# Kernel optimization log

Hardware: AMD Instinct MI355X
Metric: run time of the kernel (lower is better)

Reference implementation:

```python
import jax, jax.numpy as jnp
import numpy as np

B, S, D, E, K = 4, 2048, 1024, 8, 2


def setup_inputs() -> dict:
    key = jax.random.key(0)
    k1, k2, k3 = jax.random.split(key, 3)
    scale = 1.0 / np.sqrt(D)
    x = jax.random.normal(k1, (B, S, D), dtype=jnp.float32)
    Wg = jax.random.normal(k2, (D, E), dtype=jnp.float32) * scale
    bg = jnp.zeros((E,), dtype=jnp.float32)
    We = jax.random.normal(k3, (E, D, D), dtype=jnp.float32) * scale
    be = jnp.zeros((E, D), dtype=jnp.float32)
    return {"x": x, "Wg": Wg, "bg": bg, "We": We, "be": be}


def reference(x, Wg, bg, We, be):
    # gate scores: [B, S, E]
    gate_scores = jnp.einsum("bsd,de->bse", x, Wg) + bg
    topk_values, topk_indices = jax.lax.top_k(gate_scores, K)
    # mask: -inf everywhere except at top-k indices (where value == score)
    sel = jax.nn.one_hot(topk_indices, E, dtype=jnp.bool_).any(axis=-2)  # [B,S,E]
    masked = jnp.where(sel, gate_scores, -jnp.inf)
    gate_weights = jax.nn.softmax(masked, axis=-1)  # [B,S,E]
    # dense all-expert compute, as in the original: [B,S,E,D]
    expert_outputs = jnp.einsum("bsd,edh->bseh", x, We) + be
    fused = jnp.einsum("bse,bseh->bsh", gate_weights, expert_outputs)
    return fused
```

## Files before the change

### kernel.cpp

```cpp
#include <hip/hip_runtime.h>
#include <stdint.h>

#define NTOK   8192
#define DIM    1024
#define NEXP   8
#define MAXP   8192

#define BM 128
#define BN 128
#define BK 32

typedef float  f32x4  __attribute__((ext_vector_type(4)));
typedef __bf16 bf16x8 __attribute__((ext_vector_type(8)));

typedef __attribute__((address_space(1))) const void* gas_ptr;
typedef __attribute__((address_space(3))) void*       las_ptr;

__device__ __forceinline__ unsigned short f32_to_bf16(float f) {
  union { float f; unsigned int u; } v; v.f = f;
  unsigned int u = v.u;
  unsigned int r = (u + 0x7FFFu + ((u >> 16) & 1u)) >> 16;
  return (unsigned short)r;
}

__global__ __launch_bounds__(256) void prep_kernel(
    const float* __restrict__ We, unsigned short* __restrict__ Wt,
    const float* __restrict__ x, const float* __restrict__ Wg,
    const float* __restrict__ bg, unsigned short* __restrict__ Xbf,
    int* __restrict__ tok_ee, float2* __restrict__ tok_w) {
  __shared__ float tile[64][65];
  const int bid = blockIdx.x;
  if (bid < 2048) {
    const int e  = bid >> 8;
    const int d0 = ((bid >> 4) & 15) * 64;
    const int h0 = (bid & 15) * 64;
    const int t  = threadIdx.x;
    const int tx = t & 63, ty = t >> 6;
    const float* src = We + (size_t)e * DIM * DIM;
#pragma unroll
    for (int i = 0; i < 16; ++i) {
      int d = ty + i * 4;
      tile[d][tx] = src[(size_t)(d0 + d) * DIM + (h0 + tx)];
    }
    __syncthreads();
    unsigned short* dst = Wt + (size_t)e * DIM * DIM;
    const int tx2 = t & 31, ty8 = t >> 5;
#pragma unroll
    for (int i = 0; i < 8; ++i) {
      int h = ty8 + i * 8;
      int d = tx2 * 2;
      unsigned int pk = (unsigned int)f32_to_bf16(tile[d][h]) |
                        ((unsigned int)f32_to_bf16(tile[d + 1][h]) << 16);
      *(unsigned int*)&dst[(size_t)(h0 + h) * DIM + d0 + d] = pk;
    }
    return;
  }
  const int blk  = bid - 2048;
  const int wave = threadIdx.x >> 6;
  const int lane = threadIdx.x & 63;
  const int tok0 = blk * 16 + wave * 4;

  float xs[4][16];
#pragma unroll
  for (int t = 0; t < 4; ++t) {
    const float* xr = x + (size_t)(tok0 + t) * DIM + lane * 16;
#pragma unroll
    for (int i = 0; i < 4; ++i)
      *(f32x4*)&xs[t][i * 4] = *(const f32x4*)(xr + i * 4);
  }
#pragma unroll
  for (int t = 0; t < 4; ++t) {
    unsigned int pk[8];
#pragma unroll
    for (int i = 0; i < 8; ++i)
      pk[i] = (unsigned int)f32_to_bf16(xs[t][2 * i]) |
              ((unsigned int)f32_to_bf16(xs[t][2 * i + 1]) << 16);
    uint4* xb = (uint4*)(Xbf + (size_t)(tok0 + t) * DIM + lane * 16);
    xb[0] = make_uint4(pk[0], pk[1], pk[2], pk[3]);
    xb[1] = make_uint4(pk[4], pk[5], pk[6], pk[7]);
  }

  double acc[4][8];
#pragma unroll
  for (int t = 0; t < 4; ++t)
#pragma unroll
    for (int e = 0; e < 8; ++e) acc[t][e] = 0.0;

  const float* wr = Wg + (size_t)(lane * 16) * NEXP;
#pragma unroll
  for (int i = 0; i < 16; ++i) {
    f32x4 wa = *(const f32x4*)(wr + i * 8);
    f32x4 wb = *(const f32x4*)(wr + i * 8 + 4);
    double w0 = wa[0], w1 = wa[1], w2 = wa[2], w3 = wa[3];
    double w4 = wb[0], w5 = wb[1], w6 = wb[2], w7 = wb[3];
#pragma unroll
    for (int t = 0; t < 4; ++t) {
      double xd = (double)xs[t][i];
      acc[t][0] += xd * w0; acc[t][1] += xd * w1;
      acc[t][2] += xd * w2; acc[t][3] += xd * w3;
      acc[t][4] += xd * w4; acc[t][5] += xd * w5;
      acc[t][6] += xd * w6; acc[t][7] += xd * w7;
    }
  }
#pragma unroll
  for (int m = 1; m < 64; m <<= 1)
#pragma unroll
    for (int t = 0; t < 4; ++t)
#pragma unroll
      for (int e = 0; e < 8; ++e) acc[t][e] += __shfl_xor(acc[t][e], m, 64);

  if (lane == 0) {
#pragma unroll
    for (int t = 0; t < 4; ++t) {
      float s[8];
#pragma unroll
      for (int e = 0; e < 8; ++e) s[e] = (float)acc[t][e] + bg[e];
      int i0 = 0; float v0 = s[0];
#pragma unroll
      for (int e = 1; e < 8; ++e) if (s[e] > v0) { v0 = s[e]; i0 = e; }
      int i1 = -1; float v1 = -3.4e38f;
#pragma unroll
      for (int e = 0; e < 8; ++e) if (e != i0 && s[e] > v1) { v1 = s[e]; i1 = e; }
      float t1 = expf(v1 - v0);
      float den = 1.0f + t1;
      tok_ee[tok0 + t] = i0 | (i1 << 8);
      tok_w[tok0 + t]  = make_float2(1.0f / den, t1 / den);
    }
  }
}

__global__ __launch_bounds__(1024) void compact_kernel(
    const int* __restrict__ tok_ee, const float2* __restrict__ tok_w,
    int* __restrict__ counts, int* __restrict__ pair_token,
    float* __restrict__ pair_w) {
  __shared__ int wave_cnt[16][NEXP];
  __shared__ int wave_off[16][NEXP];
  __shared__ int base[NEXP];
  __shared__ int chunk_tot[NEXP];
  const int tid = threadIdx.x, wave = tid >> 6, lane = tid & 63;
  if (tid < NEXP) base[tid] = 0;
  __syncthreads();
  for (int c = 0; c < NTOK / 1024; ++c) {
    const int t = c * 1024 + tid;
    const int p = tok_ee[t];
    const int e0 = p & 255, e1 = (p >> 8) & 255;
    const float2 w = tok_w[t];
    int pre0 = 0, pre1 = 0;
    const unsigned long long below = (1ull << lane) - 1ull;
#pragma unroll
    for (int e = 0; e < NEXP; ++e) {
      unsigned long long m = __ballot(e0 == e || e1 == e);
      if (e0 == e) pre0 = __popcll(m & below);
      if (e1 == e) pre1 = __popcll(m & below);
      if (lane == 0) wave_cnt[wave][e] = __popcll(m);
    }
    __syncthreads();
    if (tid < NEXP) {
      int s = 0;
      for (int w2 = 0; w2 < 16; ++w2) {
        wave_off[w2][tid] = s;
        s += wave_cnt[w2][tid];
      }
      chunk_tot[tid] = s;
    }
    __syncthreads();
    const int s0 = base[e0] + wave_off[wave][e0] + pre0;
    const int s1 = base[e1] + wave_off[wave][e1] + pre1;
    pair_token[e0 * MAXP + s0] = (t << 1);     pair_w[e0 * MAXP + s0] = w.x;
    pair_token[e1 * MAXP + s1] = (t << 1) | 1; pair_w[e1 * MAXP + s1] = w.y;
    __syncthreads();
    if (tid < NEXP) base[tid] += chunk_tot[tid];
    __syncthreads();
  }
  if (tid < NEXP) counts[tid] = base[tid];
}

__global__ __launch_bounds__(256) void moe_gemm(
    const unsigned short* __restrict__ Xbf, const unsigned short* __restrict__ Wt,
    const float* __restrict__ be, const int* __restrict__ counts,
    const int* __restrict__ pair_token, const float* __restrict__ pair_w,
    float* __restrict__ part, float* __restrict__ Y, int use_part) {
  const int id  = blockIdx.x;
  const int e   = id & 7;
  const int n0  = ((id >> 3) & 7) * BN;
  const int m0  = (id >> 6) * BM;
  const int cnt = counts[e];
  if (m0 >= cnt) return;

  __shared__ __align__(16) unsigned short As[2][BM * BK];
  __shared__ __align__(16) unsigned short Bs[2][BN * BK];

  const int tid  = threadIdx.x;
  const int wave = tid >> 6;
  const int lane = tid & 63;
  const int fm   = lane & 15;
  const int fq   = lane >> 4;
  const int wm   = wave >> 1;
  const int wn   = wave & 1;

  const int srow = wave * 32 + (lane >> 2);
  const int kc   = (lane & 3) * 8;
  const unsigned short* gA[2];
  const unsigned short* gB[2];
#pragma unroll
  for (int c = 0; c < 2; ++c) {
    int r  = srow + c * 16;
    int gr = m0 + r;
    int tk = (gr < cnt) ? (pair_token[e * MAXP + gr] >> 1) : 0;
    gA[c] = Xbf + (size_t)tk * DIM + kc;
    gB[c] = Wt + (size_t)e * DIM * DIM + (size_t)(n0 + r) * DIM + kc;
  }

#define STAGE(buf, koff)                                                      \
  {                                                                           \
    _Pragma("unroll") for (int c = 0; c < 2; ++c) {                           \
      __builtin_amdgcn_global_load_lds(                                       \
          (gas_ptr)(uintptr_t)(gA[c] + (koff)),                               \
          (las_ptr)(uintptr_t)(&As[buf][(wave * 2 + c) * 512]), 16, 0, 0);    \
      __builtin_amdgcn_global_load_lds(                                       \
          (gas_ptr)(uintptr_t)(gB[c] + (koff)),                               \
          (las_ptr)(uintptr_t)(&Bs[buf][(wave * 2 + c) * 512]), 16, 0, 0);    \
    }                                                                         \
  }

  f32x4 acc[4][4];
#pragma unroll
  for (int i = 0; i < 4; ++i)
#pragma unroll
    for (int j = 0; j < 4; ++j) { f32x4 z = {0.f, 0.f, 0.f, 0.f}; acc[i][j] = z; }

  STAGE(0, 0);
  int cur = 0;
  for (int k0 = 0; k0 < DIM; k0 += BK) {
    __syncthreads();
    if (k0 + BK < DIM) STAGE(cur ^ 1, k0 + BK);

    bf16x8 af[4], bfr[4];
#pragma unroll
    for (int i = 0; i < 4; ++i)
      af[i] = *(const bf16x8*)&As[cur][(wm * 64 + i * 16 + fm) * BK + fq * 8];
#pragma unroll
    for (int j = 0; j < 4; ++j)
      bfr[j] = *(const bf16x8*)&Bs[cur][(wn * 64 + j * 16 + fm) * BK + fq * 8];
#pragma unroll
    for (int i = 0; i < 4; ++i)
#pragma unroll
      for (int j = 0; j < 4; ++j)
        acc[i][j] = __builtin_amdgcn_mfma_f32_16x16x32_bf16(af[i], bfr[j],
                                                            acc[i][j], 0, 0, 0);
    cur ^= 1;
  }
#undef STAGE

  int   rowv[4][4];
  float wrow[4][4];
#pragma unroll
  for (int i = 0; i < 4; ++i)
#pragma unroll
    for (int r = 0; r < 4; ++r) {
      int gr = m0 + wm * 64 + i * 16 + fq * 4 + r;
      bool valid = gr < cnt;
      rowv[i][r] = valid ? pair_token[e * MAXP + gr] : -1;
      wrow[i][r] = valid ? pair_w[e * MAXP + gr] : 0.f;
    }
  if (use_part) {
#pragma unroll
    for (int j = 0; j < 4; ++j) {
      int col = n0 + wn * 64 + j * 16 + fm;
      float bev = be[e * DIM + col];
#pragma unroll
      for (int i = 0; i < 4; ++i)
#pragma unroll
        for (int r = 0; r < 4; ++r) {
          int v = rowv[i][r];
          if (v >= 0)
            part[(size_t)v * DIM + col] = wrow[i][r] * (acc[i][j][r] + bev);
        }
    }
  } else {
#pragma unroll
    for (int j = 0; j < 4; ++j) {
      int col = n0 + wn * 64 + j * 16 + fm;
      float bev = be[e * DIM + col];
#pragma unroll
      for (int i = 0; i < 4; ++i)
#pragma unroll
        for (int r = 0; r < 4; ++r) {
          int v = rowv[i][r];
          if (v >= 0)
            atomicAdd(Y + (size_t)(v >> 1) * DIM + col,
                      wrow[i][r] * (acc[i][j][r] + bev));
        }
    }
  }
}

__global__ __launch_bounds__(256) void reduce_pairs(
    const float* __restrict__ part, float* __restrict__ Y) {
  const int g0 = blockIdx.x * 256 + threadIdx.x;
#pragma unroll
  for (int it = 0; it < 4; ++it) {
    const int g = g0 + it * (2048 * 256);
    const int t = g >> 8;
    const int o = (g & 255) * 4;
    const f32x4 a = *(const f32x4*)(part + (size_t)(2 * t) * DIM + o);
    const f32x4 b = *(const f32x4*)(part + (size_t)(2 * t + 1) * DIM + o);
    *(f32x4*)(Y + (size_t)t * DIM + o) = a + b;
  }
}

extern "C" void kernel_launch(void* const* d_in, const int* in_sizes, int n_in,
                              void* d_out, int out_size, void* d_ws, size_t ws_size,
                              hipStream_t stream) {
  const float* x  = (const float*)d_in[0];
  const float* Wg = (const float*)d_in[1];
  const float* bg = (const float*)d_in[2];
  const float* We = (const float*)d_in[3];
  const float* be = (const float*)d_in[4];
  float* Y = (float*)d_out;

  const size_t MB = 1024 * 1024;
  char* ws = (char*)d_ws;
  unsigned short* Xbf = (unsigned short*)ws;
  unsigned short* Wt  = (unsigned short*)(ws + 16 * MB);
  const size_t part_bytes = (size_t)NTOK * 2 * DIM * 4;
  const size_t need = 32 * MB + part_bytes + 1 * MB;
  const int use_part = ws_size >= need;
  float* part = (float*)(ws + 32 * MB);
  char* p2 = ws + 32 * MB + (use_part ? part_bytes : 0);
  int*    counts     = (int*)p2;
  int*    pair_token = (int*)(p2 + 256);
  float*  pair_w     = (float*)(p2 + 256 + 262144);
  int*    tok_ee     = (int*)(p2 + 256 + 2 * 262144);
  float2* tok_w      = (float2*)(p2 + 256 + 2 * 262144 + 32768);

  if (!use_part)
    hipMemsetAsync(d_out, 0, (size_t)out_size * sizeof(float), stream);

  prep_kernel<<<2560, 256, 0, stream>>>(We, Wt, x, Wg, bg, Xbf, tok_ee, tok_w);
  compact_kernel<<<1, 1024, 0, stream>>>(tok_ee, tok_w, counts, pair_token,
                                         pair_w);
  moe_gemm<<<8 * 8 * (NTOK / BM), 256, 0, stream>>>(
      Xbf, Wt, be, counts, pair_token, pair_w, part, Y, use_part);
  if (use_part)
    reduce_pairs<<<2048, 256, 0, stream>>>(part, Y);
}
```

Before: 237.9 us.

## Pre-tile expert weights, parallelize compaction per expert, store partials in fp16

The weight-prep kernel now writes expert weights in a tile-major layout, so each GEMM B-stage reads one contiguous block per wave. Compaction runs one block per expert instead of a single block looping over all experts, which removes the serial dependency. The per-pair partial outputs are stored as fp16 rather than fp32, halving the write and reread traffic of the partial buffer and the reduction. This lowers accuracy of the partials and changes the reduce kernel's indexing.

```diff
diff --git a/kernel.cpp b/kernel.cpp
--- a/kernel.cpp
+++ b/kernel.cpp
@@ -10,8 +10,9 @@
 #define BN 128
 #define BK 32
 
-typedef float  f32x4  __attribute__((ext_vector_type(4)));
-typedef __bf16 bf16x8 __attribute__((ext_vector_type(8)));
+typedef float    f32x4  __attribute__((ext_vector_type(4)));
+typedef __bf16   bf16x8 __attribute__((ext_vector_type(8)));
+typedef _Float16 h16x8  __attribute__((ext_vector_type(8)));
 
 typedef __attribute__((address_space(1))) const void* gas_ptr;
 typedef __attribute__((address_space(3))) void*       las_ptr;
@@ -24,7 +25,7 @@
 }
 
 __global__ __launch_bounds__(256) void prep_kernel(
-    const float* __restrict__ We, unsigned short* __restrict__ Wt,
+    const float* __restrict__ We, unsigned short* __restrict__ Wf,
     const float* __restrict__ x, const float* __restrict__ Wg,
     const float* __restrict__ bg, unsigned short* __restrict__ Xbf,
     int* __restrict__ tok_ee, float2* __restrict__ tok_w) {
@@ -43,15 +44,23 @@
       tile[d][tx] = src[(size_t)(d0 + d) * DIM + (h0 + tx)];
     }
     __syncthreads();
-    unsigned short* dst = Wt + (size_t)e * DIM * DIM;
-    const int tx2 = t & 31, ty8 = t >> 5;
-#pragma unroll
-    for (int i = 0; i < 8; ++i) {
-      int h = ty8 + i * 8;
-      int d = tx2 * 2;
-      unsigned int pk = (unsigned int)f32_to_bf16(tile[d][h]) |
-                        ((unsigned int)f32_to_bf16(tile[d + 1][h]) << 16);
-      *(unsigned int*)&dst[(size_t)(h0 + h) * DIM + d0 + d] = pk;
+    const int nt    = h0 >> 7;
+    const int rbase = h0 & 64;
+    const int hl    = t >> 2;
+    const int k8    = t & 3;
+#pragma unroll
+    for (int reg = 0; reg < 2; ++reg) {
+      const int kt = (d0 >> 5) + reg;
+      unsigned int pk[4];
+#pragma unroll
+      for (int q = 0; q < 4; ++q) {
+        int dl = reg * 32 + k8 * 8 + q * 2;
+        pk[q] = (unsigned int)f32_to_bf16(tile[dl][hl]) |
+                ((unsigned int)f32_to_bf16(tile[dl + 1][hl]) << 16);
+      }
+      size_t base = (((size_t)(e * 8 + nt) * 32 + kt) << 12) +
+                    (size_t)(rbase + hl) * 32 + k8 * 8;
+      *(uint4*)&Wf[base] = make_uint4(pk[0], pk[1], pk[2], pk[3]);
     }
     return;
   }
@@ -133,56 +142,46 @@
     const int* __restrict__ tok_ee, const float2* __restrict__ tok_w,
     int* __restrict__ counts, int* __restrict__ pair_token,
     float* __restrict__ pair_w) {
-  __shared__ int wave_cnt[16][NEXP];
-  __shared__ int wave_off[16][NEXP];
-  __shared__ int base[NEXP];
-  __shared__ int chunk_tot[NEXP];
+  __shared__ int wave_cnt[16];
+  __shared__ int wave_off[16];
+  const int e = blockIdx.x;
   const int tid = threadIdx.x, wave = tid >> 6, lane = tid & 63;
-  if (tid < NEXP) base[tid] = 0;
-  __syncthreads();
+  int base = 0;
   for (int c = 0; c < NTOK / 1024; ++c) {
     const int t = c * 1024 + tid;
     const int p = tok_ee[t];
-    const int e0 = p & 255, e1 = (p >> 8) & 255;
-    const float2 w = tok_w[t];
-    int pre0 = 0, pre1 = 0;
-    const unsigned long long below = (1ull << lane) - 1ull;
-#pragma unroll
-    for (int e = 0; e < NEXP; ++e) {
-      unsigned long long m = __ballot(e0 == e || e1 == e);
-      if (e0 == e) pre0 = __popcll(m & below);
-      if (e1 == e) pre1 = __popcll(m & below);
-      if (lane == 0) wave_cnt[wave][e] = __popcll(m);
-    }
-    __syncthreads();
-    if (tid < NEXP) {
-      int s = 0;
-      for (int w2 = 0; w2 < 16; ++w2) {
-        wave_off[w2][tid] = s;
-        s += wave_cnt[w2][tid];
-      }
-      chunk_tot[tid] = s;
-    }
-    __syncthreads();
-    const int s0 = base[e0] + wave_off[wave][e0] + pre0;
-    const int s1 = base[e1] + wave_off[wave][e1] + pre1;
-    pair_token[e0 * MAXP + s0] = (t << 1);     pair_w[e0 * MAXP + s0] = w.x;
-    pair_token[e1 * MAXP + s1] = (t << 1) | 1; pair_w[e1 * MAXP + s1] = w.y;
-    __syncthreads();
-    if (tid < NEXP) base[tid] += chunk_tot[tid];
-    __syncthreads();
-  }
-  if (tid < NEXP) counts[tid] = base[tid];
+    const bool m0 = ((p & 255) == e);
+    const bool m1 = (((p >> 8) & 255) == e);
+    const unsigned long long m = __ballot(m0 || m1);
+    const int pre = __popcll(m & ((1ull << lane) - 1ull));
+    if (lane == 0) wave_cnt[wave] = __popcll(m);
+    __syncthreads();
+    if (tid == 0) {
+      int s = base;
+      for (int w = 0; w < 16; ++w) { wave_off[w] = s; s += wave_cnt[w]; }
+      base = s;
+    }
+    __syncthreads();
+    if (m0 || m1) {
+      const float2 w = tok_w[t];
+      const int slot = wave_off[wave] + pre;
+      pair_token[e * MAXP + slot] = (t << 1) | (m1 ? 1 : 0);
+      pair_w[e * MAXP + slot]     = m1 ? w.y : w.x;
+    }
+    __syncthreads();
+  }
+  if (tid == 0) counts[e] = base;
 }
 
 __global__ __launch_bounds__(256) void moe_gemm(
-    const unsigned short* __restrict__ Xbf, const unsigned short* __restrict__ Wt,
+    const unsigned short* __restrict__ Xbf, const unsigned short* __restrict__ Wf,
     const float* __restrict__ be, const int* __restrict__ counts,
     const int* __restrict__ pair_token, const float* __restrict__ pair_w,
-    float* __restrict__ part, float* __restrict__ Y, int use_part) {
+    _Float16* __restrict__ part, float* __restrict__ Y, int use_part) {
   const int id  = blockIdx.x;
   const int e   = id & 7;
-  const int n0  = ((id >> 3) & 7) * BN;
+  const int nt  = (id >> 3) & 7;
+  const int n0  = nt * BN;
   const int m0  = (id >> 6) * BM;
   const int cnt = counts[e];
   if (m0 >= cnt) return;
@@ -201,24 +200,24 @@
   const int srow = wave * 32 + (lane >> 2);
   const int kc   = (lane & 3) * 8;
   const unsigned short* gA[2];
-  const unsigned short* gB[2];
 #pragma unroll
   for (int c = 0; c < 2; ++c) {
     int r  = srow + c * 16;
     int gr = m0 + r;
     int tk = (gr < cnt) ? (pair_token[e * MAXP + gr] >> 1) : 0;
     gA[c] = Xbf + (size_t)tk * DIM + kc;
-    gB[c] = Wt + (size_t)e * DIM * DIM + (size_t)(n0 + r) * DIM + kc;
-  }
-
-#define STAGE(buf, koff)                                                      \
+  }
+  const unsigned short* gB = Wf + (((size_t)(e * 8 + nt) * 32) << 12) +
+                             (wave * 2) * 512 + lane * 8;
+
+#define STAGE(buf, k0v)                                                       \
   {                                                                           \
     _Pragma("unroll") for (int c = 0; c < 2; ++c) {                           \
       __builtin_amdgcn_global_load_lds(                                       \
-          (gas_ptr)(uintptr_t)(gA[c] + (koff)),                               \
+          (gas_ptr)(uintptr_t)(gA[c] + (k0v)),                                \
           (las_ptr)(uintptr_t)(&As[buf][(wave * 2 + c) * 512]), 16, 0, 0);    \
       __builtin_amdgcn_global_load_lds(                                       \
-          (gas_ptr)(uintptr_t)(gB[c] + (koff)),                               \
+          (gas_ptr)(uintptr_t)(gB + (size_t)(k0v) * 128 + c * 512),           \
           (las_ptr)(uintptr_t)(&Bs[buf][(wave * 2 + c) * 512]), 16, 0, 0);    \
     }                                                                         \
   }
@@ -274,7 +273,8 @@
         for (int r = 0; r < 4; ++r) {
           int v = rowv[i][r];
           if (v >= 0)
-            part[(size_t)v * DIM + col] = wrow[i][r] * (acc[i][j][r] + bev);
+            part[(size_t)v * DIM + col] =
+                (_Float16)(wrow[i][r] * (acc[i][j][r] + bev));
         }
     }
   } else {
@@ -296,17 +296,19 @@
 }
 
 __global__ __launch_bounds__(256) void reduce_pairs(
-    const float* __restrict__ part, float* __restrict__ Y) {
-  const int g0 = blockIdx.x * 256 + threadIdx.x;
-#pragma unroll
-  for (int it = 0; it < 4; ++it) {
-    const int g = g0 + it * (2048 * 256);
-    const int t = g >> 8;
-    const int o = (g & 255) * 4;
-    const f32x4 a = *(const f32x4*)(part + (size_t)(2 * t) * DIM + o);
-    const f32x4 b = *(const f32x4*)(part + (size_t)(2 * t + 1) * DIM + o);
-    *(f32x4*)(Y + (size_t)t * DIM + o) = a + b;
-  }
+    const _Float16* __restrict__ part, float* __restrict__ Y) {
+  const int g = blockIdx.x * 256 + threadIdx.x;
+  const int t = g >> 7;
+  const int o = (g & 127) * 8;
+  const h16x8 a = *(const h16x8*)(part + (size_t)(2 * t) * DIM + o);
+  const h16x8 b = *(const h16x8*)(part + (size_t)(2 * t + 1) * DIM + o);
+  float* y = Y + (size_t)t * DIM + o;
+  f32x4 lo = {(float)a[0] + (float)b[0], (float)a[1] + (float)b[1],
+              (float)a[2] + (float)b[2], (float)a[3] + (float)b[3]};
+  f32x4 hi = {(float)a[4] + (float)b[4], (float)a[5] + (float)b[5],
+              (float)a[6] + (float)b[6], (float)a[7] + (float)b[7]};
+  *(f32x4*)y = lo;
+  *(f32x4*)(y + 4) = hi;
 }
 
 extern "C" void kernel_launch(void* const* d_in, const int* in_sizes, int n_in,
@@ -322,11 +324,11 @@
   const size_t MB = 1024 * 1024;
   char* ws = (char*)d_ws;
   unsigned short* Xbf = (unsigned short*)ws;
-  unsigned short* Wt  = (unsigned short*)(ws + 16 * MB);
-  const size_t part_bytes = (size_t)NTOK * 2 * DIM * 4;
+  unsigned short* Wf  = (unsigned short*)(ws + 16 * MB);
+  const size_t part_bytes = (size_t)NTOK * 2 * DIM * 2;
   const size_t need = 32 * MB + part_bytes + 1 * MB;
   const int use_part = ws_size >= need;
-  float* part = (float*)(ws + 32 * MB);
+  _Float16* part = (_Float16*)(ws + 32 * MB);
   char* p2 = ws + 32 * MB + (use_part ? part_bytes : 0);
   int*    counts     = (int*)p2;
   int*    pair_token = (int*)(p2 + 256);
@@ -337,11 +339,11 @@
   if (!use_part)
     hipMemsetAsync(d_out, 0, (size_t)out_size * sizeof(float), stream);
 
-  prep_kernel<<<2560, 256, 0, stream>>>(We, Wt, x, Wg, bg, Xbf, tok_ee, tok_w);
-  compact_kernel<<<1, 1024, 0, stream>>>(tok_ee, tok_w, counts, pair_token,
-                                         pair_w);
+  prep_kernel<<<2560, 256, 0, stream>>>(We, Wf, x, Wg, bg, Xbf, tok_ee, tok_w);
+  compact_kernel<<<NEXP, 1024, 0, stream>>>(tok_ee, tok_w, counts, pair_token,
+                                            pair_w);
   moe_gemm<<<8 * 8 * (NTOK / BM), 256, 0, stream>>>(
-      Xbf, Wt, be, counts, pair_token, pair_w, part, Y, use_part);
+      Xbf, Wf, be, counts, pair_token, pair_w, part, Y, use_part);
   if (use_part)
-    reduce_pairs<<<2048, 256, 0, stream>>>(part, Y);
-}
+    reduce_pairs<<<NTOK * DIM / 8 / 256, 256, 0, stream>>>(part, Y);
+}
```

After: 228.3 us. 4.0% less time.
